# Performance work log

Measured on AMD Instinct MI355X. Metric: run time of the kernel, lower is better.

Reference implementation:

```python
import jax, jax.numpy as jnp
import numpy as np

W = 0.5  # loss weight from __init__
EPS = 1e-14


def gradient_l2_loss(x):
    """Mean squared forward finite-difference along each spatial axis of (B,s,r,c)."""
    loss = 0.0
    for ax in (1, 2, 3):
        d = jnp.diff(x, axis=ax)
        loss = loss + jnp.mean(d * d)
    return loss


def setup_inputs() -> dict:
    key = jax.random.key(0)
    k1, k2 = jax.random.split(key)
    B, S, R, C = 2, 128, 128, 128
    L = jax.random.normal(k1, (B, 3, S, R, C), dtype=jnp.float32)
    U = jax.random.normal(k2, (B, 9, S, R, C), dtype=jnp.float32)
    return {"L": L, "U": U}


def reference(L, U):
    B, _, S, R, C = U.shape
    # torch.sort(L, dim=1, descending=True) -> indices[:,0] == argmax over the 3 eigenvalues
    idx0 = jnp.argmax(L, axis=1)  # (B,S,R,C) int
    # U channel layout U{row}_{col}: reshape to (B, col=3, row=3, S,R,C)
    Uview = U.reshape(B, 3, 3, S, R, C)
    idx = jnp.broadcast_to(idx0[:, None, None], (B, 3, 1, S, R, C))
    # faithful to original gather(dim=2)[:, :, 0]
    major = jnp.take_along_axis(Uview, idx, axis=2)[:, :, 0]  # (B,3,S,R,C)
    am = jnp.abs(major)
    den = jnp.sum(am * am, axis=1)  # (B,S,R,C)
    den = jnp.where(den < EPS, EPS, den)
    e1, e2, e3 = am[:, 0], am[:, 1], am[:, 2]
    CO = jnp.sqrt(0.5 * ((e1 - e2) ** 2 + (e2 - e3) ** 2 + (e3 - e1) ** 2) / den)
    CO_grad = 0.0
    for i in range(9):  # fixed small channel loop
        CO_grad = CO_grad + gradient_l2_loss(U[:, i])
    return (CO + CO_grad).mean() * W
```

## Files before the change

### kernel.cpp

```cpp
#include <hip/hip_runtime.h>

#define SS 128
#define RR 128
#define CC 128
#define EPSF 1e-14f

__global__ __launch_bounds__(256, 2) void scol_main(const float* __restrict__ L,
                                                    const float* __restrict__ U,
                                                    float4* __restrict__ part) {
    const int SRC = SS * RR * CC;

    int tid = threadIdx.x;
    int c4  = tid & 31;
    int row = blockIdx.x * 8 + (tid >> 5);
    int r   = row & (RR - 1);
    int sr  = row >> 7;
    int s   = sr & (SS - 1);
    int b   = sr >> 7;
    int c   = c4 << 2;

    int pos    = (row - b * (SS * RR)) * CC + c;
    int base_l = b * 3 * SRC + pos;
    int base_u = b * 9 * SRC + pos;

    bool  hr = (r < RR - 1), hs = (s < SS - 1), hc = (c4 < 31);
    float wr = hr ? 1.f : 0.f;
    float ws = hs ? 1.f : 0.f;
    float wc = hc ? 1.f : 0.f;
    int offr = hr ? CC : 0;
    int offs = hs ? RR * CC : 0;

    float4 l0 = *(const float4*)(L + base_l);
    float4 l1 = *(const float4*)(L + base_l + SRC);
    float4 l2 = *(const float4*)(L + base_l + 2 * SRC);

    float4 u[9], ur[9], us[9];
#pragma unroll
    for (int ch = 0; ch < 9; ++ch) {
        const float* p = U + base_u + ch * SRC;
        u[ch] = *(const float4*)(p);
    }
#pragma unroll
    for (int ch = 0; ch < 9; ++ch) {
        const float* p = U + base_u + ch * SRC;
        ur[ch] = *(const float4*)(p + offr);
        us[ch] = *(const float4*)(p + offs);
    }

    float L0[4] = {l0.x, l0.y, l0.z, l0.w};
    float L1[4] = {l1.x, l1.y, l1.z, l1.w};
    float L2[4] = {l2.x, l2.y, l2.z, l2.w};
    int idx[4];
#pragma unroll
    for (int j = 0; j < 4; ++j) {
        int id = 0;
        float best = L0[j];
        if (L1[j] > best) { best = L1[j]; id = 1; }
        if (L2[j] > best) { best = L2[j]; id = 2; }
        idx[j] = id;
    }

    float am[3][4];
#pragma unroll
    for (int g = 0; g < 3; ++g)
#pragma unroll
        for (int j = 0; j < 4; ++j) am[g][j] = 0.f;

    float a_dc = 0.f, t_dcb = 0.f, t_dr = 0.f, t_ds = 0.f;

#pragma unroll
    for (int ch = 0; ch < 9; ++ch) {
        float4 uu = u[ch];
        float uuv[4] = {uu.x, uu.y, uu.z, uu.w};
        int g = ch / 3, m = ch % 3;
#pragma unroll
        for (int j = 0; j < 4; ++j)
            if (idx[j] == m) am[g][j] = fabsf(uuv[j]);

        float d;
        d = uu.y - uu.x; a_dc += d * d;
        d = uu.z - uu.y; a_dc += d * d;
        d = uu.w - uu.z; a_dc += d * d;
        float un = __shfl_down(uu.x, 1);
        d = un - uu.w; t_dcb += d * d;

        float4 R4 = ur[ch];
        d = R4.x - uu.x; t_dr += d * d;
        d = R4.y - uu.y; t_dr += d * d;
        d = R4.z - uu.z; t_dr += d * d;
        d = R4.w - uu.w; t_dr += d * d;

        float4 S4 = us[ch];
        d = S4.x - uu.x; t_ds += d * d;
        d = S4.y - uu.y; t_ds += d * d;
        d = S4.z - uu.z; t_ds += d * d;
        d = S4.w - uu.w; t_ds += d * d;
    }
    a_dc += wc * t_dcb;
    float a_dr = wr * t_dr;
    float a_ds = ws * t_ds;

    float a_co = 0.f;
#pragma unroll
    for (int j = 0; j < 4; ++j) {
        float e1 = am[0][j], e2 = am[1][j], e3 = am[2][j];
        float den = e1 * e1 + e2 * e2 + e3 * e3;
        den = fmaxf(den, EPSF);
        float num = 0.5f * ((e1 - e2) * (e1 - e2) + (e2 - e3) * (e2 - e3) +
                            (e3 - e1) * (e3 - e1));
        a_co += sqrtf(num / den);
    }

#pragma unroll
    for (int off = 32; off > 0; off >>= 1) {
        a_co += __shfl_down(a_co, off);
        a_ds += __shfl_down(a_ds, off);
        a_dr += __shfl_down(a_dr, off);
        a_dc += __shfl_down(a_dc, off);
    }

    __shared__ float s_co[4], s_ds[4], s_dr[4], s_dc[4];
    int wid  = threadIdx.x >> 6;
    int lane = threadIdx.x & 63;
    if (lane == 0) {
        s_co[wid] = a_co; s_ds[wid] = a_ds;
        s_dr[wid] = a_dr; s_dc[wid] = a_dc;
    }
    __syncthreads();
    if (threadIdx.x == 0) {
        float t_co = 0.f, t_s = 0.f, t_r = 0.f, t_c = 0.f;
        for (int w = 0; w < 4; ++w) {
            t_co += s_co[w]; t_s += s_ds[w];
            t_r += s_dr[w]; t_c += s_dc[w];
        }
        part[blockIdx.x] = make_float4(t_co, t_s, t_r, t_c);
    }
}

__global__ __launch_bounds__(256) void scol_final(const float4* __restrict__ part,
                                                  float* __restrict__ out,
                                                  int nblk, int B) {
    double d_co = 0., d_ds = 0., d_dr = 0., d_dc = 0.;
    for (int i = threadIdx.x; i < nblk; i += blockDim.x) {
        float4 p = part[i];
        d_co += (double)p.x; d_ds += (double)p.y;
        d_dr += (double)p.z; d_dc += (double)p.w;
    }
#pragma unroll
    for (int off = 32; off > 0; off >>= 1) {
        d_co += __shfl_down(d_co, off);
        d_ds += __shfl_down(d_ds, off);
        d_dr += __shfl_down(d_dr, off);
        d_dc += __shfl_down(d_dc, off);
    }
    __shared__ double sh[4][4];
    int wid  = threadIdx.x >> 6;
    int lane = threadIdx.x & 63;
    if (lane == 0) {
        sh[wid][0] = d_co; sh[wid][1] = d_ds;
        sh[wid][2] = d_dr; sh[wid][3] = d_dc;
    }
    __syncthreads();
    if (threadIdx.x == 0) {
        double t_co = 0., t_ds = 0., t_dr = 0., t_dc = 0.;
        for (int w = 0; w < 4; ++w) {
            t_co += sh[w][0]; t_ds += sh[w][1];
            t_dr += sh[w][2]; t_dc += sh[w][3];
        }
        double nvox = (double)B * SS * RR * CC;
        double nds  = (double)B * (SS - 1) * RR * CC;
        double ndr  = (double)B * SS * (RR - 1) * CC;
        double ndc  = (double)B * SS * RR * (CC - 1);
        out[0] = (float)(0.5 * (t_co / nvox + t_ds / nds + t_dr / ndr + t_dc / ndc));
    }
}

extern "C" void kernel_launch(void* const* d_in, const int* in_sizes, int n_in,
                              void* d_out, int out_size, void* d_ws, size_t ws_size,
                              hipStream_t stream) {
    const float* L = (const float*)d_in[0];
    const float* U = (const float*)d_in[1];
    float* out = (float*)d_out;

    int B = in_sizes[1] / (9 * SS * RR * CC);
    int nrow = B * SS * RR;
    int blocks = nrow / 8;

    float4* part = (float4*)d_ws;

    hipLaunchKernelGGL(scol_main, dim3(blocks), dim3(256), 0, stream,
                       L, U, part);
    hipLaunchKernelGGL(scol_final, dim3(1), dim3(256), 0, stream,
                       part, out, blocks, B);
}
```

Baseline: 242.8 us.

## March each block along slices to reuse previous slice for s-gradient

Each block now processes 4 consecutive S-slices of an 8-row tile, keeping the previous slice's 9 channel values in registers for the s-direction difference instead of reloading the neighbor slice. This cuts the redundant us[] loads, which were a full extra read of U. Block IDs are also swizzled across groups of 8, and launch bounds are raised to 4 waves per SIMD. The trade-off is fewer blocks with a serial inner loop, and a dependency on gridDim being divisible by 8 for the swizzle.

```diff
diff --git a/kernel.cpp b/kernel.cpp
--- a/kernel.cpp
+++ b/kernel.cpp
@@ -3,112 +3,132 @@
 #define SS 128
 #define RR 128
 #define CC 128
+#define SCH 4
 #define EPSF 1e-14f
 
-__global__ __launch_bounds__(256, 2) void scol_main(const float* __restrict__ L,
+__global__ __launch_bounds__(256, 4) void scol_main(const float* __restrict__ L,
                                                     const float* __restrict__ U,
                                                     float4* __restrict__ part) {
     const int SRC = SS * RR * CC;
+    const int RC  = RR * CC;
+
+    int bid = blockIdx.x;
+    int cpx = gridDim.x >> 3;
+    int swz = (bid & 7) * cpx + (bid >> 3);
+
+    int rt = swz & 15;
+    int sc = (swz >> 4) & 31;
+    int b  = swz >> 9;
 
     int tid = threadIdx.x;
-    int c4  = tid & 31;
-    int row = blockIdx.x * 8 + (tid >> 5);
-    int r   = row & (RR - 1);
-    int sr  = row >> 7;
-    int s   = sr & (SS - 1);
-    int b   = sr >> 7;
-    int c   = c4 << 2;
-
-    int pos    = (row - b * (SS * RR)) * CC + c;
-    int base_l = b * 3 * SRC + pos;
-    int base_u = b * 9 * SRC + pos;
-
-    bool  hr = (r < RR - 1), hs = (s < SS - 1), hc = (c4 < 31);
+    int c4       = tid & 31;
+    int rowLocal = tid >> 5;
+    int r  = (rt << 3) + rowLocal;
+    int s0 = sc * SCH;
+    int c  = c4 << 2;
+
+    bool hr = (r < RR - 1), hc = (c4 < 31);
     float wr = hr ? 1.f : 0.f;
-    float ws = hs ? 1.f : 0.f;
     float wc = hc ? 1.f : 0.f;
     int offr = hr ? CC : 0;
-    int offs = hs ? RR * CC : 0;
-
-    float4 l0 = *(const float4*)(L + base_l);
-    float4 l1 = *(const float4*)(L + base_l + SRC);
-    float4 l2 = *(const float4*)(L + base_l + 2 * SRC);
-
-    float4 u[9], ur[9], us[9];
-#pragma unroll
-    for (int ch = 0; ch < 9; ++ch) {
-        const float* p = U + base_u + ch * SRC;
-        u[ch] = *(const float4*)(p);
-    }
-#pragma unroll
-    for (int ch = 0; ch < 9; ++ch) {
-        const float* p = U + base_u + ch * SRC;
-        ur[ch] = *(const float4*)(p + offr);
-        us[ch] = *(const float4*)(p + offs);
-    }
-
-    float L0[4] = {l0.x, l0.y, l0.z, l0.w};
-    float L1[4] = {l1.x, l1.y, l1.z, l1.w};
-    float L2[4] = {l2.x, l2.y, l2.z, l2.w};
-    int idx[4];
-#pragma unroll
-    for (int j = 0; j < 4; ++j) {
-        int id = 0;
-        float best = L0[j];
-        if (L1[j] > best) { best = L1[j]; id = 1; }
-        if (L2[j] > best) { best = L2[j]; id = 2; }
-        idx[j] = id;
-    }
-
-    float am[3][4];
-#pragma unroll
-    for (int g = 0; g < 3; ++g)
-#pragma unroll
-        for (int j = 0; j < 4; ++j) am[g][j] = 0.f;
-
-    float a_dc = 0.f, t_dcb = 0.f, t_dr = 0.f, t_ds = 0.f;
-
-#pragma unroll
-    for (int ch = 0; ch < 9; ++ch) {
-        float4 uu = u[ch];
-        float uuv[4] = {uu.x, uu.y, uu.z, uu.w};
-        int g = ch / 3, m = ch % 3;
-#pragma unroll
-        for (int j = 0; j < 4; ++j)
-            if (idx[j] == m) am[g][j] = fabsf(uuv[j]);
-
-        float d;
-        d = uu.y - uu.x; a_dc += d * d;
-        d = uu.z - uu.y; a_dc += d * d;
-        d = uu.w - uu.z; a_dc += d * d;
-        float un = __shfl_down(uu.x, 1);
-        d = un - uu.w; t_dcb += d * d;
-
-        float4 R4 = ur[ch];
-        d = R4.x - uu.x; t_dr += d * d;
-        d = R4.y - uu.y; t_dr += d * d;
-        d = R4.z - uu.z; t_dr += d * d;
-        d = R4.w - uu.w; t_dr += d * d;
-
-        float4 S4 = us[ch];
-        d = S4.x - uu.x; t_ds += d * d;
-        d = S4.y - uu.y; t_ds += d * d;
-        d = S4.z - uu.z; t_ds += d * d;
-        d = S4.w - uu.w; t_ds += d * d;
-    }
-    a_dc += wc * t_dcb;
-    float a_dr = wr * t_dr;
-    float a_ds = ws * t_ds;
-
-    float a_co = 0.f;
-#pragma unroll
-    for (int j = 0; j < 4; ++j) {
-        float e1 = am[0][j], e2 = am[1][j], e3 = am[2][j];
-        float den = e1 * e1 + e2 * e2 + e3 * e3;
-        den = fmaxf(den, EPSF);
-        float num = 0.5f * ((e1 - e2) * (e1 - e2) + (e2 - e3) * (e2 - e3) +
-                            (e3 - e1) * (e3 - e1));
-        a_co += sqrtf(num / den);
+
+    int pos = (s0 * RR + r) * CC + c;
+    const float* Ub = U + (size_t)b * 9 * SRC + pos;
+    const float* Lb = L + (size_t)b * 3 * SRC + pos;
+
+    float a_dc = 0.f, a_dr = 0.f, a_ds = 0.f, a_co = 0.f;
+
+    float4 prev[9];
+#pragma unroll
+    for (int ch = 0; ch < 9; ++ch)
+        prev[ch] = *(const float4*)(Ub + ch * SRC);
+
+#pragma unroll 1
+    for (int ss = 0; ss < SCH; ++ss) {
+        const float* Up = Ub + ss * RC;
+        const float* Lp = Lb + ss * RC;
+
+        float4 l0 = *(const float4*)(Lp);
+        float4 l1 = *(const float4*)(Lp + SRC);
+        float4 l2 = *(const float4*)(Lp + 2 * SRC);
+        float L0v[4] = {l0.x, l0.y, l0.z, l0.w};
+        float L1v[4] = {l1.x, l1.y, l1.z, l1.w};
+        float L2v[4] = {l2.x, l2.y, l2.z, l2.w};
+        int idx[4];
+#pragma unroll
+        for (int j = 0; j < 4; ++j) {
+            int id = 0;
+            float best = L0v[j];
+            if (L1v[j] > best) { best = L1v[j]; id = 1; }
+            if (L2v[j] > best) { best = L2v[j]; id = 2; }
+            idx[j] = id;
+        }
+
+        float am[3][4];
+#pragma unroll
+        for (int g = 0; g < 3; ++g)
+#pragma unroll
+            for (int j = 0; j < 4; ++j) am[g][j] = 0.f;
+
+        float t_dcb = 0.f, t_dr = 0.f;
+
+#pragma unroll
+        for (int ch = 0; ch < 9; ++ch) {
+            float4 uu = *(const float4*)(Up + ch * SRC);
+            float4 vr = *(const float4*)(Up + ch * SRC + offr);
+            float4 pv = prev[ch];
+
+            int g = ch / 3, m = ch % 3;
+            float uuv[4] = {uu.x, uu.y, uu.z, uu.w};
+#pragma unroll
+            for (int j = 0; j < 4; ++j)
+                if (idx[j] == m) am[g][j] = fabsf(uuv[j]);
+
+            float d;
+            d = uu.y - uu.x; a_dc += d * d;
+            d = uu.z - uu.y; a_dc += d * d;
+            d = uu.w - uu.z; a_dc += d * d;
+            float un = __shfl_down(uu.x, 1);
+            d = un - uu.w; t_dcb += d * d;
+
+            d = vr.x - uu.x; t_dr += d * d;
+            d = vr.y - uu.y; t_dr += d * d;
+            d = vr.z - uu.z; t_dr += d * d;
+            d = vr.w - uu.w; t_dr += d * d;
+
+            d = uu.x - pv.x; a_ds += d * d;
+            d = uu.y - pv.y; a_ds += d * d;
+            d = uu.z - pv.z; a_ds += d * d;
+            d = uu.w - pv.w; a_ds += d * d;
+
+            prev[ch] = uu;
+        }
+        a_dc += wc * t_dcb;
+        a_dr += wr * t_dr;
+
+#pragma unroll
+        for (int j = 0; j < 4; ++j) {
+            float e1 = am[0][j], e2 = am[1][j], e3 = am[2][j];
+            float den = e1 * e1 + e2 * e2 + e3 * e3;
+            den = fmaxf(den, EPSF);
+            float num = 0.5f * ((e1 - e2) * (e1 - e2) + (e2 - e3) * (e2 - e3) +
+                                (e3 - e1) * (e3 - e1));
+            a_co += sqrtf(num / den);
+        }
+    }
+
+    if (s0 + SCH < SS) {
+        const float* Up = Ub + SCH * RC;
+#pragma unroll
+        for (int ch = 0; ch < 9; ++ch) {
+            float4 uu = *(const float4*)(Up + ch * SRC);
+            float4 pv = prev[ch];
+            float d;
+            d = uu.x - pv.x; a_ds += d * d;
+            d = uu.y - pv.y; a_ds += d * d;
+            d = uu.z - pv.z; a_ds += d * d;
+            d = uu.w - pv.w; a_ds += d * d;
+        }
     }
 
 #pragma unroll
@@ -183,8 +203,7 @@
     float* out = (float*)d_out;
 
     int B = in_sizes[1] / (9 * SS * RR * CC);
-    int nrow = B * SS * RR;
-    int blocks = nrow / 8;
+    int blocks = B * (SS / SCH) * (RR / 8);
 
     float4* part = (float4*)d_ws;
 
```

Result: slower. 250.6 us (+3.2%).
